# Kernel optimization log

Measured on AMD Instinct MI355X. Metric: run time of the kernel, lower is better.

## Reference

```python
import jax, jax.numpy as jnp
import numpy as np

D_MODEL = 768
N_HEADS = 12
HEAD_DIM = D_MODEL // N_HEADS


def setup_inputs() -> dict:
    key = jax.random.key(0)
    k_x, k_wqkv, k_bqkv, k_wp, k_bp = jax.random.split(key, 5)
    s = 1.0 / np.sqrt(D_MODEL)
    return {
        "x": jax.random.normal(k_x, (8, 1024, D_MODEL), dtype=jnp.float32),
        "w_qkv": jax.random.uniform(k_wqkv, (D_MODEL, 3 * D_MODEL), jnp.float32, -s, s),
        "b_qkv": jax.random.uniform(k_bqkv, (3 * D_MODEL,), jnp.float32, -s, s),
        "w_proj": jax.random.uniform(k_wp, (D_MODEL, D_MODEL), jnp.float32, -s, s),
        "b_proj": jax.random.uniform(k_bp, (D_MODEL,), jnp.float32, -s, s),
    }


def reference(x, w_qkv, b_qkv, w_proj, b_proj):
    # x: [B, N, D]. Dropout is identity in eval mode.
    B, N, D = x.shape
    qkv = x @ w_qkv + b_qkv  # [B, N, 3D]
    qkv = qkv.reshape(B, N, 3, N_HEADS, HEAD_DIM).transpose(2, 0, 3, 1, 4)
    q, k, v = qkv[0], qkv[1], qkv[2]  # each [B, H, N, hd]
    scale = 1.0 / np.sqrt(HEAD_DIM).astype(np.float32)
    attn = jnp.einsum("bhqd,bhkd->bhqk", q, k) * scale  # [B, H, N, N]
    attn = jax.nn.softmax(attn, axis=-1)
    out = jnp.einsum("bhqk,bhkd->bhqd", attn, v)  # [B, H, N, hd]
    out = out.transpose(0, 2, 1, 3).reshape(B, N, D)
    return out @ w_proj + b_proj
```

## Files before the change

### kernel.cpp

```cpp
#include <hip/hip_runtime.h>
#include <math.h>

#define D_MODEL 768
#define NHEADS  12
#define HDIM    64
#define SEQ     1024
#define BATCH   8
#define NBH     (BATCH*NHEADS)
#define M_TOTAL (BATCH*SEQ)
#define KT_D    (D_MODEL/32)
#define QKV_COLS (3*D_MODEL)

typedef __attribute__((ext_vector_type(8))) short bf16x8;
typedef __attribute__((ext_vector_type(4))) float f32x4;

#define MFMA16(a,b,c) __builtin_amdgcn_mfma_f32_16x16x32_bf16((a),(b),(c),0,0,0)

#define QSCALE 0.18033688011112042f

__device__ inline unsigned short f2bf(float f) {
    unsigned u = __float_as_uint(f);
    u += 0x7FFFu + ((u >> 16) & 1u);
    return (unsigned short)(u >> 16);
}
__device__ inline float bf2f(unsigned short h) {
    return __uint_as_float(((unsigned)h) << 16);
}
__device__ inline void gload16(const void* g, const void* l) {
    __builtin_amdgcn_global_load_lds(
        (const __attribute__((address_space(1))) unsigned*)g,
        (__attribute__((address_space(3))) unsigned*)l, 16, 0, 0);
}
__device__ inline float exp2_fast(float x) {
#if __has_builtin(__builtin_amdgcn_exp2f)
    return __builtin_amdgcn_exp2f(x);
#else
    float r; asm("v_exp_f32 %0, %1" : "=v"(r) : "v"(x)); return r;
#endif
}


#define NA_TOT 786432
#define NB1_TOT 221184
#define NB2_TOT 73728

__global__ __launch_bounds__(256)
void convert_all(const float* __restrict__ x,    unsigned short* __restrict__ Xf,
                 const float* __restrict__ wq,   unsigned short* __restrict__ Wq,
                 const float* __restrict__ wp,   unsigned short* __restrict__ Wp)
{
    const int gid = blockIdx.x * 256 + threadIdx.x;
    const int lane = gid & 63;
    if (gid < NA_TOT) {
        const int sub = gid >> 6;
        const int kt = sub % KT_D;
        const int mt = sub / KT_D;
        const float* s = x + (size_t)(mt*16 + (lane & 15)) * D_MODEL + kt*32 + (lane >> 4)*8;
        float4 v0 = *(const float4*)(s);
        float4 v1 = *(const float4*)(s + 4);
        float vv[8] = {v0.x, v0.y, v0.z, v0.w, v1.x, v1.y, v1.z, v1.w};
        union { unsigned short u[8]; bf16x8 v; } H;
        #pragma unroll
        for (int i = 0; i < 8; ++i) H.u[i] = f2bf(vv[i]);
        *(bf16x8*)(Xf + (size_t)sub * 512 + lane * 8) = H.v;
    } else {
        const float* src;
        unsigned short* dst;
        int sub, ldN;
        if (gid < NA_TOT + NB1_TOT) {
            src = wq; dst = Wq; ldN = QKV_COLS; sub = (gid - NA_TOT) >> 6;
        } else if (gid < NA_TOT + NB1_TOT + NB2_TOT) {
            src = wp; dst = Wp; ldN = D_MODEL; sub = (gid - NA_TOT - NB1_TOT) >> 6;
        } else {
            return;
        }
        const int kt = sub % KT_D;
        const int nt = sub / KT_D;
        const int n  = nt*16 + (lane & 15);
        const int k0 = kt*32 + (lane >> 4)*8;
        const float* s = src + (size_t)k0 * ldN + n;
        union { unsigned short u[8]; bf16x8 v; } H;
        #pragma unroll
        for (int i = 0; i < 8; ++i) H.u[i] = f2bf(s[(size_t)i * ldN]);
        *(bf16x8*)(dst + (size_t)sub * 512 + lane * 8) = H.v;
    }
}

template<int MODE>
__global__ __launch_bounds__(MODE == 0 ? 512 : 256, 4)
void gemm_frag(const unsigned short* __restrict__ Af,
               const unsigned short* __restrict__ Bf,
               const float* __restrict__ bias,
               float* __restrict__ outF,
               unsigned short* __restrict__ outQ,
               unsigned short* __restrict__ outK,
               unsigned short* __restrict__ outV)
{
    constexpr int NW     = (MODE == 0) ? 8 : 4;
    constexpr int NSUB_N = (MODE == 0) ? 8 : 4;
    constexpr int ACH    = 8;
    constexpr int NCH    = ACH + NSUB_N;
    __shared__ unsigned short Asm[ACH * 512];
    __shared__ unsigned short Bsm[NSUB_N * 512];
    const int t = threadIdx.x, lane = t & 63, wid = t >> 6;
    const int wr = (MODE == 0) ? (wid >> 2) : (wid >> 1);
    const int wc = (MODE == 0) ? (wid & 3)  : (wid & 1);
    const int bid = blockIdx.x;
    const int mb = (bid & 7) * 8 + ((bid >> 3) & 7);
    const int nb = bid >> 6;

    f32x4 acc[4][2] = {};

    for (int kt = 0; kt < KT_D; ++kt) {
        __syncthreads();
        #pragma unroll
        for (int i = 0; i < NCH/NW; ++i) {
            const int c = wid * (NCH/NW) + i;
            if (c < ACH) {
                const unsigned short* g =
                    Af + ((size_t)(mb*8 + c)*KT_D + kt)*512 + lane*8;
                gload16(g, (const char*)Asm + (size_t)c*1024);
            } else {
                const int j = c - ACH;
                const unsigned short* g =
                    Bf + ((size_t)(nb*NSUB_N + j)*KT_D + kt)*512 + lane*8;
                gload16(g, (const char*)Bsm + (size_t)j*1024);
            }
        }
        __syncthreads();

        bf16x8 bh[2];
        #pragma unroll
        for (int n = 0; n < 2; ++n)
            bh[n] = *(const bf16x8*)(Bsm + (wc*2 + n)*512 + lane*8);
        bf16x8 ah[4];
        #pragma unroll
        for (int m = 0; m < 4; ++m)
            ah[m] = *(const bf16x8*)(Asm + (wr*4 + m)*512 + lane*8);
        #pragma unroll
        for (int m = 0; m < 4; ++m)
            #pragma unroll
            for (int n = 0; n < 2; ++n)
                acc[m][n] = MFMA16(ah[m], bh[n], acc[m][n]);
    }

    const int rowW = mb*128 + wr*64;
    const int colW = nb*(NSUB_N*16) + wc*32;
    if (MODE == 1) {
        #pragma unroll
        for (int m = 0; m < 4; ++m)
            #pragma unroll
            for (int n = 0; n < 2; ++n) {
                const int col = colW + n*16 + (lane & 15);
                const float bv = bias[col];
                #pragma unroll
                for (int r = 0; r < 4; ++r) {
                    const int row = rowW + m*16 + (lane >> 4)*4 + r;
                    outF[(size_t)row * D_MODEL + col] = acc[m][n][r] + bv;
                }
            }
    } else {
        const int which = colW / D_MODEL;
        const int h     = (colW % D_MODEL) >> 6;
        #pragma unroll
        for (int m = 0; m < 4; ++m)
            #pragma unroll
            for (int n = 0; n < 2; ++n) {
                const int col = colW + n*16 + (lane & 15);
                const int d = col & 63;
                const float bv = bias[col];
                #pragma unroll
                for (int r = 0; r < 4; ++r) {
                    const int row = rowW + m*16 + (lane >> 4)*4 + r;
                    const int b = row >> 10, sq = row & 1023;
                    float val = acc[m][n][r] + bv;
                    if (which <= 1) {
                        if (which == 0) val *= QSCALE;
                        const int sub = (sq >> 4)*2 + (d >> 5);
                        const int lp  = (sq & 15) + (((d & 31) >> 3) << 4);
                        unsigned short* dst = (which == 0) ? outQ : outK;
                        dst[(size_t)(b*NHEADS + h)*65536
                            + (size_t)sub*512 + lp*8 + (d & 7)] = f2bf(val);
                    } else {
                        const int sub = (d >> 4)*32 + (sq >> 5);
                        const int lp  = (d & 15) + (((sq & 31) >> 3) << 4);
                        outV[(size_t)(b*NHEADS + h)*65536
                             + (size_t)sub*512 + lp*8 + (sq & 7)] = f2bf(val);
                    }
                }
            }
    }
}

__global__ __launch_bounds__(512, 6)
void attn_frag(const unsigned short* __restrict__ Qf,
               const unsigned short* __restrict__ Kf,
               const unsigned short* __restrict__ Vf,
               unsigned short* __restrict__ Cf)
{
    __shared__ unsigned short Ksm[2][8 * 512];
    __shared__ unsigned short Vsm[2][8 * 512];
    __shared__ unsigned short Psm[8 * 1024];

    const int t = threadIdx.x, lane = t & 63, wid = t >> 6;
    const int bid = blockIdx.x;
    const int qb  = (bid >> 3) & 7;
    const int bh  = (bid & 7) * 12 + (bid >> 6);
    const int mt0 = qb*8 + wid;
    const size_t kBase = (size_t)bh * 65536;

    const int slot  = lane & 7;
    const int colg  = (lane & 15) >> 3;
    const int qrow0 = (lane >> 4) * 4;

    auto stage = [&](int b, int jt) {
        #pragma unroll
        for (int i = 0; i < 2; ++i) {
            const int ch = wid*2 + i;
            if (ch < 8) {
                const unsigned short* gk = Kf + kBase + (size_t)(jt*8 + ch)*512;
                gload16(gk + lane*8, (const char*)&Ksm[b][0] + (size_t)ch*1024);
            } else {
                const int cv = ch - 8;
                const unsigned short* gv = Vf + kBase
                    + (size_t)((cv >> 1)*32 + jt*2 + (cv & 1))*512;
                gload16(gv + lane*8, (const char*)&Vsm[b][0] + (size_t)cv*1024);
            }
        }
    };

    stage(0, 0);

    bf16x8 qh[2];
    #pragma unroll
    for (int kt = 0; kt < 2; ++kt)
        qh[kt] = *(const bf16x8*)(Qf + kBase + ((size_t)mt0*2 + kt)*512 + lane*8);

    bf16x8 ones;
    #pragma unroll
    for (int i = 0; i < 8; ++i) ones[i] = (short)0x3F80;

    f32x4 out[4] = {};
    f32x4 lacc = {};
    float m_run[4];
    #pragma unroll
    for (int r = 0; r < 4; ++r) m_run[r] = -INFINITY;

    unsigned short* Pw = Psm + wid * 1024;

    __syncthreads();

    for (int jt = 0; jt < 16; ++jt) {
        const int cur = jt & 1;
        if (jt + 1 < 16) stage(cur ^ 1, jt + 1);

        f32x4 s[4] = {};
        #pragma unroll
        for (int jn = 0; jn < 4; ++jn)
            #pragma unroll
            for (int kt = 0; kt < 2; ++kt) {
                const bf16x8 kh = *(const bf16x8*)(&Ksm[cur][0] + (jn*2 + kt)*512 + lane*8);
                s[jn] = MFMA16(qh[kt], kh, s[jn]);
            }

        float mx[4];
        int ok = 1;
        #pragma unroll
        for (int r = 0; r < 4; ++r) {
            const float v = fmaxf(fmaxf(s[0][r], s[1][r]), fmaxf(s[2][r], s[3][r]));
            mx[r] = v;
            ok &= (v <= m_run[r] + 8.0f);
        }
        if (!__all(ok)) {
            float alf[4];
            #pragma unroll
            for (int r = 0; r < 4; ++r) {
                float v = mx[r];
                #pragma unroll
                for (int msk = 1; msk < 16; msk <<= 1)
                    v = fmaxf(v, __shfl_xor(v, msk));
                const float mn = fmaxf(m_run[r], v);
                alf[r] = exp2_fast(m_run[r] - mn);
                m_run[r] = mn;
            }
            #pragma unroll
            for (int dt = 0; dt < 4; ++dt)
                #pragma unroll
                for (int r = 0; r < 4; ++r)
                    out[dt][r] *= alf[r];
            #pragma unroll
            for (int r = 0; r < 4; ++r)
                lacc[r] *= alf[r];
        }

        #pragma unroll
        for (int r = 0; r < 4; ++r) {
            const float mb_ = m_run[r];
            const int tl   = qrow0 + r + (colg << 4);
            const int idxb = ((tl << 3) | slot) ^ (tl & 0x18);
            #pragma unroll
            for (int jn = 0; jn < 4; ++jn) {
                const float e = exp2_fast(s[jn][r] - mb_);
                Pw[(jn >> 1)*512 + idxb + ((jn & 1) << 8)]
                    = (unsigned short)(__float_as_uint(e) >> 16);
            }
        }

        const int rdswz = (lane*8) ^ (lane & 0x18);
        #pragma unroll
        for (int kt2 = 0; kt2 < 2; ++kt2) {
            const bf16x8 pa = *(const bf16x8*)(Pw + kt2*512 + rdswz);
            #pragma unroll
            for (int dt = 0; dt < 4; ++dt) {
                const bf16x8 vh = *(const bf16x8*)(&Vsm[cur][0] + (dt*2 + kt2)*512 + lane*8);
                out[dt] = MFMA16(pa, vh, out[dt]);
            }
            lacc = MFMA16(pa, ones, lacc);
        }

        __syncthreads();
    }

    const int b = bh / NHEADS, h = bh % NHEADS;
    #pragma unroll
    for (int r = 0; r < 4; ++r) {
        const float inv = 1.0f / lacc[r];
        const int sq = mt0*16 + qrow0 + r;
        const int mrow = b*SEQ + sq;
        #pragma unroll
        for (int dt = 0; dt < 4; ++dt) {
            const int c = h*64 + dt*16 + (lane & 15);
            const float val = out[dt][r] * inv;
            Cf[((size_t)(mrow >> 4)*KT_D + (c >> 5))*512
               + ((mrow & 15) + (((c & 31) >> 3) << 4))*8 + (c & 7)] = f2bf(val);
        }
    }
}

extern "C" void kernel_launch(void* const* d_in, const int* in_sizes, int n_in,
                              void* d_out, int out_size, void* d_ws, size_t ws_size,
                              hipStream_t stream)
{
    const float* x      = (const float*)d_in[0];
    const float* w_qkv  = (const float*)d_in[1];
    const float* b_qkv  = (const float*)d_in[2];
    const float* w_proj = (const float*)d_in[3];
    const float* b_proj = (const float*)d_in[4];
    float* out = (float*)d_out;

    unsigned short* ws = (unsigned short*)d_ws;
    unsigned short* Xf = ws;
    unsigned short* Wq = Xf + 6291456;
    unsigned short* Wp = Wq + 1769472;
    unsigned short* Qf = Wp + 589824;
    unsigned short* Kf = Qf + 6291456;
    unsigned short* Vf = Kf + 6291456;
    unsigned short* Cf = Vf + 6291456;

    convert_all<<<dim3(4224), 256, 0, stream>>>(x, Xf, w_qkv, Wq, w_proj, Wp);

    gemm_frag<0><<<dim3(1152), 512, 0, stream>>>(Xf, Wq, b_qkv, nullptr, Qf, Kf, Vf);
    attn_frag<<<dim3(768), 512, 0, stream>>>(Qf, Kf, Vf, Cf);
    gemm_frag<1><<<dim3(768), 256, 0, stream>>>(Cf, Wp, b_proj, out,
                                                nullptr, nullptr, nullptr);
}
```

Measured before the change: 120.8 us.

## Triple-buffer GEMM shared-memory tiles with async prefetch two steps ahead

```diff
diff --git a/kernel.cpp b/kernel.cpp
--- a/kernel.cpp
+++ b/kernel.cpp
@@ -100,8 +100,8 @@
     constexpr int NSUB_N = (MODE == 0) ? 8 : 4;
     constexpr int ACH    = 8;
     constexpr int NCH    = ACH + NSUB_N;
-    __shared__ unsigned short Asm[ACH * 512];
-    __shared__ unsigned short Bsm[NSUB_N * 512];
+    constexpr int CPW    = NCH / NW;
+    __shared__ unsigned short sm[3][NCH * 512];
     const int t = threadIdx.x, lane = t & 63, wid = t >> 6;
     const int wr = (MODE == 0) ? (wid >> 2) : (wid >> 1);
     const int wc = (MODE == 0) ? (wid & 3)  : (wid & 1);
@@ -109,34 +109,46 @@
     const int mb = (bid & 7) * 8 + ((bid >> 3) & 7);
     const int nb = bid >> 6;
 
-    f32x4 acc[4][2] = {};
-
-    for (int kt = 0; kt < KT_D; ++kt) {
-        __syncthreads();
-        #pragma unroll
-        for (int i = 0; i < NCH/NW; ++i) {
-            const int c = wid * (NCH/NW) + i;
+    auto stage = [&](int b, int ktv) {
+        #pragma unroll
+        for (int i = 0; i < CPW; ++i) {
+            const int c = wid * CPW + i;
+            const unsigned short* g;
             if (c < ACH) {
-                const unsigned short* g =
-                    Af + ((size_t)(mb*8 + c)*KT_D + kt)*512 + lane*8;
-                gload16(g, (const char*)Asm + (size_t)c*1024);
+                g = Af + ((size_t)(mb*8 + c)*KT_D + ktv)*512 + lane*8;
             } else {
                 const int j = c - ACH;
-                const unsigned short* g =
-                    Bf + ((size_t)(nb*NSUB_N + j)*KT_D + kt)*512 + lane*8;
-                gload16(g, (const char*)Bsm + (size_t)j*1024);
-            }
-        }
-        __syncthreads();
-
+                g = Bf + ((size_t)(nb*NSUB_N + j)*KT_D + ktv)*512 + lane*8;
+            }
+            gload16(g, (const char*)&sm[b][0] + (size_t)c*1024);
+        }
+    };
+
+    f32x4 acc[4][2] = {};
+
+    stage(0, 0);
+    stage(1, 1);
+
+    for (int kt = 0; kt < KT_D; ++kt) {
+        if (kt + 1 < KT_D) {
+            if (MODE == 0) asm volatile("s_waitcnt vmcnt(2)" ::: "memory");
+            else           asm volatile("s_waitcnt vmcnt(3)" ::: "memory");
+        } else {
+            asm volatile("s_waitcnt vmcnt(0)" ::: "memory");
+        }
+        __builtin_amdgcn_s_barrier();
+
+        if (kt + 2 < KT_D) stage((kt + 2) % 3, kt + 2);
+
+        const unsigned short* Lb = &sm[kt % 3][0];
         bf16x8 bh[2];
         #pragma unroll
         for (int n = 0; n < 2; ++n)
-            bh[n] = *(const bf16x8*)(Bsm + (wc*2 + n)*512 + lane*8);
+            bh[n] = *(const bf16x8*)(Lb + (ACH + wc*2 + n)*512 + lane*8);
         bf16x8 ah[4];
         #pragma unroll
         for (int m = 0; m < 4; ++m)
-            ah[m] = *(const bf16x8*)(Asm + (wr*4 + m)*512 + lane*8);
+            ah[m] = *(const bf16x8*)(Lb + (wr*4 + m)*512 + lane*8);
         #pragma unroll
         for (int m = 0; m < 4; ++m)
             #pragma unroll
```

New measurement: 114.2 us. 5.5% less time.
